# Optimization experiments

Hardware: AMD Instinct MI355X
Metric: run time of the kernel (lower is better)

The kernel has to match this reference:

```python
import jax, jax.numpy as jnp
import numpy as np

N_NODES = 30000
N_EDGES = 480000
IN_SIZE = 256
EDGE_FEAT = 32
N_TOWERS = 4
DELTA = 2.5


def setup_inputs():
    key = jax.random.key(0)
    ks = jax.random.split(key, 8)
    T, d = N_TOWERS, IN_SIZE // N_TOWERS
    m_in = 2 * d + EDGE_FEAT                 # M: Linear(2*tower_in+edge_feat -> tower_in)
    u_in = (4 * 3 + 1) * d                   # U: Linear((n_agg*n_scaler+1)*tower_in -> tower_out)
    return {
        "n_feat": jax.random.normal(ks[0], (N_NODES, IN_SIZE), jnp.float32),
        "e_feat": jax.random.normal(ks[1], (N_EDGES, EDGE_FEAT), jnp.float32),
        "src": jax.random.randint(ks[2], (N_EDGES,), 0, N_NODES),
        "dst": jax.random.randint(ks[3], (N_EDGES,), 0, N_NODES),
        "M_w": jax.random.normal(ks[4], (T, d, m_in), jnp.float32) * (1.0 / np.sqrt(m_in)),
        "M_b": jnp.zeros((T, d), jnp.float32),
        "U_w": jax.random.normal(ks[5], (T, d, u_in), jnp.float32) * (1.0 / np.sqrt(u_in)),
        "U_b": jnp.zeros((T, d), jnp.float32),
        "bn_gamma": jnp.ones((T, d), jnp.float32),
        "bn_beta": jnp.zeros((T, d), jnp.float32),
        "mix_w": jax.random.normal(ks[6], (IN_SIZE, IN_SIZE), jnp.float32) * (1.0 / np.sqrt(IN_SIZE)),
        "mix_b": jnp.zeros((IN_SIZE,), jnp.float32),
    }


def reference(n_feat, e_feat, src, dst, M_w, M_b, U_w, U_b, bn_gamma, bn_beta, mix_w, mix_b):
    N, F = n_feat.shape
    T, d, _ = M_w.shape
    E = src.shape[0]
    h = n_feat.reshape(N, T, d)                                   # towers split the feature dim
    ef = jnp.broadcast_to(e_feat[:, None, :], (E, T, e_feat.shape[1]))
    f = jnp.concatenate([h[src], h[dst], ef], axis=-1)            # [E,T,2d+ef]
    msg = jnp.einsum('eti,toi->eto', f, M_w) + M_b                # per-edge message, [E,T,d]

    deg = jax.ops.segment_sum(jnp.ones((E,), msg.dtype), dst, num_segments=N)  # in-degree
    degc = jnp.maximum(deg, 1.0)[:, None, None]
    s = jax.ops.segment_sum(msg, dst, num_segments=N)
    ssq = jax.ops.segment_sum(msg * msg, dst, num_segments=N)
    mean = s / degc
    var = jax.nn.relu(ssq / degc - mean * mean)                   # DGL aggregate_var
    std = jnp.sqrt(var + 1e-30)                                   # DGL aggregate_std
    has = (deg > 0.0)[:, None, None]
    mx = jnp.where(has, jax.ops.segment_max(msg, dst, num_segments=N), 0.0)
    mn = jnp.where(has, jax.ops.segment_min(msg, dst, num_segments=N), 0.0)
    agg = jnp.concatenate([mean, mx, mn, std], axis=-1)           # [N,T,4d]

    logd = jnp.log(deg + 1.0)
    amp = (logd / DELTA)[:, None, None]                            # amplification scaler
    att = jnp.where(deg > 0.0, DELTA / jnp.maximum(logd, 1e-12), 0.0)[:, None, None]  # attenuation
    hsc = jnp.concatenate([agg, agg * amp, agg * att], axis=-1)   # [N,T,12d]

    u_in = jnp.concatenate([h, hsc], axis=-1)                     # [N,T,13d]
    u = jnp.einsum('nti,toi->nto', u_in, U_w) + U_b               # [N,T,d]
    mu = jnp.mean(u, axis=0)
    v = jnp.mean((u - mu) ** 2, axis=0)
    u = (u - mu) / jnp.sqrt(v + 1e-5) * bn_gamma + bn_beta        # BatchNorm1d (training mode)

    h_cat = u.reshape(N, F)
    mixed = h_cat @ mix_w.T + mix_b
    mixed = jnp.where(mixed > 0, mixed, 0.01 * mixed)             # LeakyReLU mixing layer
    out = mixed + n_feat                                          # residual (in_size==out_size)
    return jax.nn.relu(out)                                       # last == 0 -> ReLU
```

## Files before the change

### kernel.cpp

```cpp
#include <hip/hip_runtime.h>
#include <math.h>

constexpr float DELTA_ = 2.5f;
#define BN_BLOCKS 512
#define NPB 8

typedef __attribute__((ext_vector_type(8))) short bf16x8;
typedef __attribute__((ext_vector_type(8))) _Float16 f16x8;
typedef __attribute__((ext_vector_type(4))) float f32x4;

__device__ inline ushort bf16h(float x){
  union { float f; unsigned u; } v; v.f = x;
  unsigned r = v.u + 0x7fffu + ((v.u >> 16) & 1u);
  return (ushort)(r >> 16);
}
__device__ inline float bf16f(ushort h){
  union { unsigned u; float f; } v; v.u = ((unsigned)h) << 16;
  return v.f;
}

__global__ __launch_bounds__(256) void k_tU(const float* __restrict__ Uw, ushort* __restrict__ Wpk2){
  int i = blockIdx.x*256 + threadIdx.x;
  if (i >= 4*192*320) return;
  int k   = i % 320;
  int col = (i/320) % 192;
  int t   = i/(320*192);
  int path = col >> 6, o = col & 63;
  float v = 0.f;
  int src = -1;
  if (k < 64){ if (path == 0) src = k; }
  else        src = k + path*256;
  if (src >= 0) v = Uw[((size_t)(t*64 + o))*832 + src];
  Wpk2[i] = bf16h(v);
}

__global__ __launch_bounds__(256) void k_tMm(const float* __restrict__ mixw, ushort* __restrict__ Wm2){
  int i = blockIdx.x*256 + threadIdx.x;
  if (i >= 256*256) return;
  Wm2[i] = bf16h(mixw[i]);
}

__global__ __launch_bounds__(256) void k_tW(const float* __restrict__ Mw, _Float16* __restrict__ Wall){
  int i = blockIdx.x*256 + threadIdx.x;
  if (i >= 4*4*3*64*8) return;
  int j     = i & 7;
  int lane  = (i >> 3) & 63;
  int slice = (i / 512) % 3;
  int cb    = (i / 1536) % 4;
  int t     = i / 6144;
  int ch = t*64 + cb*16 + (lane & 15);
  int k  = slice*32 + ((lane >> 4) & 3)*8 + j;
  int off = (k < 64) ? k : (128 + (k - 64));
  Wall[i] = (_Float16)Mw[(size_t)ch*160 + off];
}

__global__ __launch_bounds__(256) void k_hist(const int* __restrict__ dstv, int* __restrict__ cnt, int E){
  int e = blockIdx.x*256 + threadIdx.x;
  if (e < E) atomicAdd(&cnt[dstv[e]], 1);
}

__global__ __launch_bounds__(256) void k_scan1(const int* __restrict__ cnt, int* __restrict__ offs,
                                               int* __restrict__ bsum, int N){
  __shared__ int lds[256];
  int i = threadIdx.x;
  int g = blockIdx.x*256 + i;
  int v = (g < N) ? cnt[g] : 0;
  int acc = v;
  lds[i] = acc; __syncthreads();
  for (int s = 1; s < 256; s <<= 1){
    int t = (i >= s) ? lds[i - s] : 0;
    __syncthreads();
    acc += t; lds[i] = acc;
    __syncthreads();
  }
  if (g < N) offs[g] = acc - v;
  if (i == 255) bsum[blockIdx.x] = acc;
}

__global__ __launch_bounds__(256) void k_scan2(int* __restrict__ bsum, int NB){
  __shared__ int lds[256];
  int i = threadIdx.x;
  int v = (i < NB) ? bsum[i] : 0;
  int acc = v;
  lds[i] = acc; __syncthreads();
  for (int s = 1; s < 256; s <<= 1){
    int t = (i >= s) ? lds[i - s] : 0;
    __syncthreads();
    acc += t; lds[i] = acc;
    __syncthreads();
  }
  if (i < NB) bsum[i] = acc - v;
}

__global__ __launch_bounds__(256) void k_scan3(int* __restrict__ offs, const int* __restrict__ bsum, int N, int E){
  int g = blockIdx.x*256 + threadIdx.x;
  if (g < N) offs[g] += bsum[blockIdx.x];
  if (g == 0) offs[N] = E;
}

__global__ __launch_bounds__(256) void k_fill(const int* __restrict__ dstv, const int* __restrict__ offs,
                                              int* __restrict__ cur, int* __restrict__ elist, int E){
  int e = blockIdx.x*256 + threadIdx.x;
  if (e < E){
    int d = dstv[e];
    elist[offs[d] + atomicAdd(&cur[d], 1)] = e;
  }
}

__global__ __launch_bounds__(256) void k_perm(const int* __restrict__ elist, const int* __restrict__ srcv,
                                              const float* __restrict__ efeat,
                                              int* __restrict__ esrc, _Float16* __restrict__ efh, int E){
  int g = blockIdx.x*256 + threadIdx.x;
  int pos = g >> 3;
  int q   = g & 7;
  if (pos >= E) return;
  int e = elist[pos];
  if (q == 0) esrc[pos] = srcv[e];
  float4 v = *(const float4*)(efeat + (size_t)e*32 + q*4);
  union { ushort4 u; _Float16 h[4]; } cv;
  cv.h[0] = (_Float16)v.x; cv.h[1] = (_Float16)v.y;
  cv.h[2] = (_Float16)v.z; cv.h[3] = (_Float16)v.w;
  *(ushort4*)(efh + (size_t)pos*32 + q*4) = cv.u;
}

__global__ __launch_bounds__(256) void k_ab(const float* __restrict__ nf, const float* __restrict__ Mw,
                                            const float* __restrict__ Mb,
                                            _Float16* __restrict__ nfh, float* __restrict__ B,
                                            ushort* __restrict__ X2, int N){
  int c = threadIdx.x;
  int t = __builtin_amdgcn_readfirstlane(threadIdx.x >> 6);
  int d = c & 63;
  int jj = d >> 3, pp = d & 7;
  float wd[64];
  const float* row = Mw + (size_t)c*160 + 64;
#pragma unroll
  for (int k = 0; k < 64; k += 4){
    float4 b = *(const float4*)(row + k);
    wd[k]=b.x; wd[k+1]=b.y; wd[k+2]=b.z; wd[k+3]=b.w;
  }
  float bias = Mb[c];
  for (int n = blockIdx.x; n < N; n += gridDim.x){
    const float* h = nf + (size_t)n*256 + t*64;
    float sb = 0.f;
#pragma unroll
    for (int k = 0; k < 64; k += 4){
      float4 h4 = *(const float4*)(h + k);
      sb = fmaf(wd[k], h4.x, sb);
      sb = fmaf(wd[k+1], h4.y, sb);
      sb = fmaf(wd[k+2], h4.z, sb);
      sb = fmaf(wd[k+3], h4.w, sb);
    }
    B[(size_t)n*256 + c] = sb + bias;
    float v = nf[(size_t)n*256 + c];
    nfh[(size_t)n*256 + c] = (_Float16)v;
    ushort hi = bf16h(v);
    size_t base = (((size_t)n*4 + t)*40 + jj)*16;
    X2[base + pp]     = hi;
    X2[base + 8 + pp] = bf16h(v - bf16f(hi));
  }
}

__global__ __launch_bounds__(256) void k_agg(const int* __restrict__ offs, const int* __restrict__ esrc,
                                             const _Float16* __restrict__ efh,
                                             const _Float16* __restrict__ nfh, const float* __restrict__ B,
                                             const _Float16* __restrict__ Wall,
                                             ushort* __restrict__ X2, float* __restrict__ sc, int N, int E){
  __shared__ _Float16 eps[256][68];
  int tid = threadIdx.x;
  int lane = tid & 63, wv = tid >> 6;
  int li = lane & 15, kq = lane >> 4;
  int c = tid;
  int tw = c >> 6, d = c & 63;

  int n0 = blockIdx.x * NPB;
  if (n0 >= N) return;
  int n1 = n0 + NPB; if (n1 > N) n1 = N;
  int oS = offs[n0], oE = offs[n1];

  f16x8 bf[4][3];
#pragma unroll
  for (int cb = 0; cb < 4; ++cb)
#pragma unroll
    for (int sl = 0; sl < 3; ++sl)
      bf[cb][sl] = *(const f16x8*)(Wall + ((((size_t)wv*4 + cb)*3 + sl)*64 + lane)*8);

  int cur = n0;
  int curstart = oS;
  int nextoff = offs[n0 + 1];
  float s = 0.f, ss = 0.f;
  float mx = -__builtin_huge_valf(), mn = __builtin_huge_valf();

#define FINALIZE(CNT)                                                             \
  {                                                                                \
    float b = B[(size_t)cur*256 + c];                                              \
    float deg = (float)(CNT);                                                      \
    float degc = fmaxf(deg, 1.f);                                                  \
    float inv = 1.f / degc;                                                        \
    float S  = fmaf(deg, b, s);                                                    \
    float SS = fmaf(deg, b*b, fmaf(2.f*b, s, ss));                                 \
    float mean = S * inv;                                                          \
    float var  = fmaxf(SS * inv - mean*mean, 0.f);                                 \
    float sd   = sqrtf(var + 1e-30f);                                              \
    float MX = ((CNT) > 0) ? (b + mx) : 0.f;                                       \
    float MN = ((CNT) > 0) ? (b + mn) : 0.f;                                       \
    size_t xb = (((size_t)cur*4 + tw)*40)*16;                                      \
    { int kk = 64 + d;       ushort h2 = bf16h(mean);                              \
      X2[xb + (kk>>3)*16 + (kk&7)] = h2;                                           \
      X2[xb + (kk>>3)*16 + 8 + (kk&7)] = bf16h(mean - bf16f(h2)); }                \
    { int kk = 128 + d;      ushort h2 = bf16h(MX);                                \
      X2[xb + (kk>>3)*16 + (kk&7)] = h2;                                           \
      X2[xb + (kk>>3)*16 + 8 + (kk&7)] = bf16h(MX - bf16f(h2)); }                  \
    { int kk = 192 + d;      ushort h2 = bf16h(MN);                                \
      X2[xb + (kk>>3)*16 + (kk&7)] = h2;                                           \
      X2[xb + (kk>>3)*16 + 8 + (kk&7)] = bf16h(MN - bf16f(h2)); }                  \
    { int kk = 256 + d;      ushort h2 = bf16h(sd);                                \
      X2[xb + (kk>>3)*16 + (kk&7)] = h2;                                           \
      X2[xb + (kk>>3)*16 + 8 + (kk&7)] = bf16h(sd - bf16f(h2)); }                  \
    if (tid == 0){                                                                 \
      float logd = logf(deg + 1.f);                                                \
      sc[(size_t)cur*2]     = logd * (1.f / DELTA_);                               \
      sc[(size_t)cur*2 + 1] = ((CNT) > 0) ? (DELTA_ / fmaxf(logd, 1e-12f)) : 0.f;  \
    }                                                                              \
  }

  for (int w0 = oS; w0 < oE; w0 += 64){
    __syncthreads();
#pragma unroll
    for (int ch4 = 0; ch4 < 4; ++ch4){
      int pos = w0 + ch4*16 + li; if (pos > E - 1) pos = E - 1;
      int src = esrc[pos];
      const _Float16* hp = nfh + (size_t)src*256 + wv*64;
      f16x8 a0 = *(const f16x8*)(hp + kq*8);
      f16x8 a1 = *(const f16x8*)(hp + 32 + kq*8);
      f16x8 a2 = *(const f16x8*)(efh + (size_t)pos*32 + kq*8);
#pragma unroll
      for (int cb = 0; cb < 4; ++cb){
        f32x4 acc = __builtin_amdgcn_mfma_f32_16x16x32_f16(a0, bf[cb][0], (f32x4)0.f, 0, 0, 0);
        acc = __builtin_amdgcn_mfma_f32_16x16x32_f16(a1, bf[cb][1], acc, 0, 0, 0);
        acc = __builtin_amdgcn_mfma_f32_16x16x32_f16(a2, bf[cb][2], acc, 0, 0, 0);
        union { ushort4 u4; _Float16 h[4]; } st;
        st.h[0] = (_Float16)acc[0];
        st.h[1] = (_Float16)acc[1];
        st.h[2] = (_Float16)acc[2];
        st.h[3] = (_Float16)acc[3];
        *(ushort4*)(&eps[wv*64 + cb*16 + li][ch4*16 + kq*4]) = st.u4;
      }
    }
    __syncthreads();

    int wend = w0 + 64; if (wend > oE) wend = oE;
    for (int g = 0; g < 64; g += 4){
      if (w0 + g >= wend) break;
      union { ushort4 u4; _Float16 h[4]; } ld;
      ld.u4 = *(const ushort4*)(&eps[c][g]);
#pragma unroll
      for (int r = 0; r < 4; ++r){
        int idx = w0 + g + r;
        if (idx >= wend) break;
        while (idx == nextoff){
          FINALIZE(nextoff - curstart)
          curstart = nextoff;
          ++cur;
          nextoff = offs[cur + 1];
          s = 0.f; ss = 0.f;
          mx = -__builtin_huge_valf(); mn = __builtin_huge_valf();
        }
        float m = (float)ld.h[r];
        s += m;
        ss = fmaf(m, m, ss);
        mx = fmaxf(mx, m);
        mn = fminf(mn, m);
      }
    }
  }

  while (cur < n1){
    FINALIZE(nextoff - curstart)
    curstart = nextoff;
    ++cur;
    if (cur < n1) nextoff = offs[cur + 1];
    s = 0.f; ss = 0.f;
    mx = -__builtin_huge_valf(); mn = __builtin_huge_valf();
  }
#undef FINALIZE
}

__global__ __launch_bounds__(256) void k_u(const ushort* __restrict__ X2, const ushort* __restrict__ Wpk2,
                                           const float* __restrict__ sc, const float* __restrict__ Ub,
                                           float* __restrict__ uout, int Nn){
  __shared__ float su[64][68];
  int tid = threadIdx.x;
  int t   = blockIdx.y;
  int nbase = blockIdx.x*64;
  int lane = tid & 63, wv = tid >> 6;
  int li = lane & 15, kc = lane >> 4;
  int cbase = wv*48;

  f32x4 acc[4][3];
#pragma unroll
  for (int ri = 0; ri < 4; ++ri)
#pragma unroll
    for (int ci = 0; ci < 3; ++ci) acc[ri][ci] = (f32x4)0.f;

  const ushort* wb = Wpk2 + (size_t)t*192*320;

#pragma unroll 2
  for (int kt = 0; kt < 10; ++kt){
    bf16x8 ah[4], al[4], bh[3];
#pragma unroll
    for (int ri = 0; ri < 4; ++ri){
      int row = nbase + ri*16 + li;
      if (row >= Nn) row = Nn - 1;
      const ushort* ap = X2 + (((size_t)row*4 + t)*40 + kt*4 + kc)*16;
      ah[ri] = *(const bf16x8*)(ap);
      al[ri] = *(const bf16x8*)(ap + 8);
    }
#pragma unroll
    for (int ci = 0; ci < 3; ++ci){
      int col = cbase + ci*16 + li;
      bh[ci] = *(const bf16x8*)(wb + (size_t)col*320 + kt*32 + kc*8);
    }
#pragma unroll
    for (int ci = 0; ci < 3; ++ci)
#pragma unroll
      for (int ri = 0; ri < 4; ++ri){
        acc[ri][ci] = __builtin_amdgcn_mfma_f32_16x16x32_bf16(ah[ri], bh[ci], acc[ri][ci], 0, 0, 0);
        acc[ri][ci] = __builtin_amdgcn_mfma_f32_16x16x32_bf16(al[ri], bh[ci], acc[ri][ci], 0, 0, 0);
      }
  }

#define Y1_STORE(CI, OB) { _Pragma("unroll") for (int ri = 0; ri < 4; ++ri)               \
    { _Pragma("unroll") for (int r = 0; r < 4; ++r)                                        \
      su[ri*16 + kc*4 + r][(OB) + li] = acc[ri][CI][r]; } }
#define Y_ADD(CI, OB, SCOFF) { _Pragma("unroll") for (int ri = 0; ri < 4; ++ri)           \
    { _Pragma("unroll") for (int r = 0; r < 4; ++r){                                       \
      int node = ri*16 + kc*4 + r;                                                        \
      int gn = nbase + node; int gnc = (gn < Nn) ? gn : (Nn - 1);                          \
      float scl = sc[(size_t)gnc*2 + (SCOFF)];                                            \
      su[node][(OB) + li] += scl * acc[ri][CI][r]; } } }

  if (wv == 0){ Y1_STORE(0, 0)  Y1_STORE(1, 16) Y1_STORE(2, 32) }
  else if (wv == 1){ Y1_STORE(0, 48) }
  __syncthreads();
  if (wv == 1){ Y_ADD(1, 0, 0)  Y_ADD(2, 16, 0) }
  else if (wv == 2){ Y_ADD(0, 32, 0) Y_ADD(1, 48, 0) }
  __syncthreads();
  if (wv == 2){ Y_ADD(2, 0, 1) }
  else if (wv == 3){ Y_ADD(0, 16, 1) Y_ADD(1, 32, 1) Y_ADD(2, 48, 1) }
  __syncthreads();
#undef Y1_STORE
#undef Y_ADD

  for (int idx = tid; idx < 64*16; idx += 256){
    int n = idx >> 4, o4 = (idx & 15)*4;
    int gn = nbase + n;
    if (gn < Nn){
      float4 v = *(float4*)(&su[n][o4]);
      const float* ubp = Ub + t*64 + o4;
      v.x += ubp[0]; v.y += ubp[1]; v.z += ubp[2]; v.w += ubp[3];
      *(float4*)(&uout[(size_t)gn*256 + t*64 + o4]) = v;
    }
  }
}

__global__ __launch_bounds__(256) void k_bnstat(const float* __restrict__ u, float* __restrict__ part, int N){
  int c = threadIdx.x;
  int b = blockIdx.x;
  float s = 0.f, ss = 0.f;
  for (int n = b; n < N; n += gridDim.x){
    float v = u[(size_t)n*256 + c];
    s += v;
    ss = fmaf(v, v, ss);
  }
  part[(size_t)b*512 + c]       = s;
  part[(size_t)b*512 + 256 + c] = ss;
}

__global__ __launch_bounds__(256) void k_bnfin(const float* __restrict__ part, const float* __restrict__ gam,
                                               const float* __restrict__ bet, float* __restrict__ bnsc, int N){
  int c = threadIdx.x;
  float s = 0.f, ss = 0.f;
  for (int b = 0; b < BN_BLOCKS; ++b){
    s  += part[(size_t)b*512 + c];
    ss += part[(size_t)b*512 + 256 + c];
  }
  float invN = 1.f / (float)N;
  float mu  = s * invN;
  float ex2 = ss * invN;
  float var = fmaxf(ex2 - mu*mu, 0.f);
  float inv = 1.f / sqrtf(var + 1e-5f);
  float scale = gam[c] * inv;
  bnsc[c]       = scale;
  bnsc[256 + c] = bet[c] - mu*scale;
}

__global__ __launch_bounds__(256) void k_mix(const float* __restrict__ u, const ushort* __restrict__ Wm2,
                                             const float* __restrict__ bnsc,
                                             const float* __restrict__ mixb, const float* __restrict__ nf,
                                             float* __restrict__ outp, int Nn){
  int tid = threadIdx.x;
  int nbase = blockIdx.x*64;
  int lane = tid & 63, wv = tid >> 6;
  int li = lane & 15, kc = lane >> 4;

  f32x4 acc[4][4];
#pragma unroll
  for (int ri = 0; ri < 4; ++ri)
#pragma unroll
    for (int ci = 0; ci < 4; ++ci) acc[ri][ci] = (f32x4)0.f;

#pragma unroll 2
  for (int kt = 0; kt < 8; ++kt){
    int k0 = kt*32 + kc*8;
    float4 s40 = *(const float4*)(bnsc + k0);
    float4 s41 = *(const float4*)(bnsc + k0 + 4);
    float4 h40 = *(const float4*)(bnsc + 256 + k0);
    float4 h41 = *(const float4*)(bnsc + 256 + k0 + 4);
    bf16x8 ah[4], al[4], bh[4];
#pragma unroll
    for (int ri = 0; ri < 4; ++ri){
      int row = nbase + ri*16 + li;
      if (row >= Nn) row = Nn - 1;
      const float* up = u + (size_t)row*256 + k0;
      float4 v0 = *(const float4*)(up);
      float4 v1 = *(const float4*)(up + 4);
      float x[8];
      x[0] = fmaf(v0.x, s40.x, h40.x); x[1] = fmaf(v0.y, s40.y, h40.y);
      x[2] = fmaf(v0.z, s40.z, h40.z); x[3] = fmaf(v0.w, s40.w, h40.w);
      x[4] = fmaf(v1.x, s41.x, h41.x); x[5] = fmaf(v1.y, s41.y, h41.y);
      x[6] = fmaf(v1.z, s41.z, h41.z); x[7] = fmaf(v1.w, s41.w, h41.w);
      union { bf16x8 v; ushort u[8]; } hh, ll;
#pragma unroll
      for (int q = 0; q < 8; ++q){
        ushort hb = bf16h(x[q]);
        hh.u[q] = hb;
        ll.u[q] = bf16h(x[q] - bf16f(hb));
      }
      ah[ri] = hh.v;
      al[ri] = ll.v;
    }
#pragma unroll
    for (int ci = 0; ci < 4; ++ci){
      int col = wv*64 + ci*16 + li;
      bh[ci] = *(const bf16x8*)(Wm2 + (size_t)col*256 + kt*32 + kc*8);
    }
#pragma unroll
    for (int ci = 0; ci < 4; ++ci)
#pragma unroll
      for (int ri = 0; ri < 4; ++ri){
        acc[ri][ci] = __builtin_amdgcn_mfma_f32_16x16x32_bf16(ah[ri], bh[ci], acc[ri][ci], 0, 0, 0);
        acc[ri][ci] = __builtin_amdgcn_mfma_f32_16x16x32_bf16(al[ri], bh[ci], acc[ri][ci], 0, 0, 0);
      }
  }

  __syncthreads();
#pragma unroll
  for (int ri = 0; ri < 4; ++ri){
#pragma unroll
    for (int r = 0; r < 4; ++r){
      int node = ri*16 + kc*4 + r;
      int gn = nbase + node;
      if (gn < Nn){
#pragma unroll
        for (int ci = 0; ci < 4; ++ci){
          int col = wv*64 + ci*16 + li;
          float m = acc[ri][ci][r] + mixb[col];
          m = (m > 0.f) ? m : 0.01f*m;
          float o = m + nf[(size_t)gn*256 + col];
          outp[(size_t)gn*256 + col] = fmaxf(o, 0.f);
        }
      }
    }
  }
}

extern "C" void kernel_launch(void* const* d_in, const int* in_sizes, int n_in,
                              void* d_out, int out_size, void* d_ws, size_t ws_size,
                              hipStream_t stream){
  const float* nf   = (const float*)d_in[0];
  const float* ef   = (const float*)d_in[1];
  const int*   srcv = (const int*)  d_in[2];
  const int*   dstv = (const int*)  d_in[3];
  const float* Mw   = (const float*)d_in[4];
  const float* Mb   = (const float*)d_in[5];
  const float* Uw   = (const float*)d_in[6];
  const float* Ub   = (const float*)d_in[7];
  const float* gam  = (const float*)d_in[8];
  const float* bet  = (const float*)d_in[9];
  const float* mixw = (const float*)d_in[10];
  const float* mixb = (const float*)d_in[11];
  int N = in_sizes[0] / 256;
  int E = in_sizes[2];
  float* out = (float*)d_out;

  char* wp = (char*)d_ws;
  auto alloc = [&](size_t bytes){
    char* p = wp;
    wp += (bytes + 1023) & ~(size_t)1023;
    return (void*)p;
  };
  int*      cnt   = (int*)     alloc((size_t)N*4);
  int*      offs  = (int*)     alloc((size_t)(N+1)*4);
  int*      cur   = (int*)     alloc((size_t)N*4);
  int*      bsum  = (int*)     alloc(256*4);
  int*      elist = (int*)     alloc((size_t)E*4);
  int*      esrc  = (int*)     alloc((size_t)E*4);
  _Float16* efh   = (_Float16*)alloc((size_t)E*32*2);
  _Float16* nfh   = (_Float16*)alloc((size_t)N*256*2);
  float*    B     = (float*)   alloc((size_t)N*256*4);
  float*    sc    = (float*)   alloc((size_t)N*2*4);
  float*    part  = (float*)   alloc((size_t)BN_BLOCKS*512*4);
  float*    bnsc  = (float*)   alloc(512*4);
  ushort*   X2    = (ushort*)  alloc((size_t)N*4*40*16*2);
  ushort*   Wpk2  = (ushort*)  alloc((size_t)4*192*320*2);
  ushort*   Wm2   = (ushort*)  alloc((size_t)256*256*2);
  _Float16* Wall  = (_Float16*)alloc((size_t)4*4*3*64*8*2);

  hipMemsetAsync(cnt,  0, (size_t)N*4,  stream);
  hipMemsetAsync(cur,  0, (size_t)N*4,  stream);

  k_tU  <<<(4*192*320 + 255)/256, 256, 0, stream>>>(Uw, Wpk2);
  k_tMm <<<(256*256 + 255)/256, 256, 0, stream>>>(mixw, Wm2);
  k_tW  <<<(4*4*3*64*8 + 255)/256, 256, 0, stream>>>(Mw, Wall);
  k_hist<<<(E + 255)/256, 256, 0, stream>>>(dstv, cnt, E);
  k_ab  <<<2048, 256, 0, stream>>>(nf, Mw, Mb, nfh, B, X2, N);

  int NB = (N + 255)/256;
  k_scan1<<<NB, 256, 0, stream>>>(cnt, offs, bsum, N);
  k_scan2<<<1, 256, 0, stream>>>(bsum, NB);
  k_scan3<<<NB, 256, 0, stream>>>(offs, bsum, N, E);
  k_fill <<<(E + 255)/256, 256, 0, stream>>>(dstv, offs, cur, elist, E);
  k_perm <<<(E*8 + 255)/256, 256, 0, stream>>>(elist, srcv, ef, esrc, efh, E);

  k_agg<<<(N + NPB - 1)/NPB, 256, 0, stream>>>(offs, esrc, efh, nfh, B, Wall, X2, sc, N, E);

  dim3 ugrid((N + 63)/64, 4);
  k_u<<<ugrid, 256, 0, stream>>>(X2, Wpk2, sc, Ub, out, N);

  k_bnstat<<<BN_BLOCKS, 256, 0, stream>>>(out, part, N);
  k_bnfin <<<1, 256, 0, stream>>>(part, gam, bet, bnsc, N);
  k_mix  <<<(N + 63)/64, 256, 0, stream>>>(out, Wm2, bnsc, mixb, nf, out, N);
}
```

Before: 450.3 us.

## Fuse batchnorm partial statistics into the U-projection epilogue and double nodes per aggregation block

Per-block channel sums and sums of squares are computed from the shared-memory tile in k_u and written as partials. This removes the separate k_bnstat kernel that re-read the whole u tensor from global memory. k_bnfin now reduces these per-tile partials, one per 64-node block. Separately, the aggregation kernel now processes 16 nodes per block instead of 8, which changes its grid size and load balance.

```diff
diff --git a/kernel.cpp b/kernel.cpp
--- a/kernel.cpp
+++ b/kernel.cpp
@@ -2,8 +2,7 @@
 #include <math.h>
 
 constexpr float DELTA_ = 2.5f;
-#define BN_BLOCKS 512
-#define NPB 8
+#define NPB 16
 
 typedef __attribute__((ext_vector_type(8))) short bf16x8;
 typedef __attribute__((ext_vector_type(8))) _Float16 f16x8;
@@ -287,8 +286,10 @@
 
 __global__ __launch_bounds__(256) void k_u(const ushort* __restrict__ X2, const ushort* __restrict__ Wpk2,
                                            const float* __restrict__ sc, const float* __restrict__ Ub,
-                                           float* __restrict__ uout, int Nn){
+                                           float* __restrict__ uout, float* __restrict__ part,
+                                           int Nn, int NBLK){
   __shared__ float su[64][68];
+  __shared__ float pbn[2][4][64];
   int tid = threadIdx.x;
   int t   = blockIdx.y;
   int nbase = blockIdx.x*64;
@@ -361,28 +362,41 @@
       *(float4*)(&uout[(size_t)gn*256 + t*64 + o4]) = v;
     }
   }
-}
-
-__global__ __launch_bounds__(256) void k_bnstat(const float* __restrict__ u, float* __restrict__ part, int N){
+
+  {
+    int cl = tid & 63, grp = tid >> 6;
+    float ubv = Ub[t*64 + cl];
+    float ps = 0.f, pss = 0.f;
+#pragma unroll
+    for (int q = 0; q < 16; ++q){
+      int nn = grp*16 + q;
+      if (nbase + nn < Nn){
+        float v = su[nn][cl] + ubv;
+        ps += v;
+        pss = fmaf(v, v, pss);
+      }
+    }
+    pbn[0][grp][cl] = ps;
+    pbn[1][grp][cl] = pss;
+  }
+  __syncthreads();
+  if (tid < 128){
+    int which = tid >> 6, cl = tid & 63;
+    float v = pbn[which][0][cl] + pbn[which][1][cl] + pbn[which][2][cl] + pbn[which][3][cl];
+    part[((size_t)t*NBLK + blockIdx.x)*128 + which*64 + cl] = v;
+  }
+}
+
+__global__ __launch_bounds__(256) void k_bnfin(const float* __restrict__ part, const float* __restrict__ gam,
+                                               const float* __restrict__ bet, float* __restrict__ bnsc,
+                                               int N, int NBLK){
   int c = threadIdx.x;
-  int b = blockIdx.x;
+  int t = c >> 6, cl = c & 63;
   float s = 0.f, ss = 0.f;
-  for (int n = b; n < N; n += gridDim.x){
-    float v = u[(size_t)n*256 + c];
-    s += v;
-    ss = fmaf(v, v, ss);
-  }
-  part[(size_t)b*512 + c]       = s;
-  part[(size_t)b*512 + 256 + c] = ss;
-}
-
-__global__ __launch_bounds__(256) void k_bnfin(const float* __restrict__ part, const float* __restrict__ gam,
-                                               const float* __restrict__ bet, float* __restrict__ bnsc, int N){
-  int c = threadIdx.x;
-  float s = 0.f, ss = 0.f;
-  for (int b = 0; b < BN_BLOCKS; ++b){
-    s  += part[(size_t)b*512 + c];
-    ss += part[(size_t)b*512 + 256 + c];
+  for (int b = 0; b < NBLK; ++b){
+    const float* pp = part + ((size_t)t*NBLK + b)*128;
+    s  += pp[cl];
+    ss += pp[64 + cl];
   }
   float invN = 1.f / (float)N;
   float mu  = s * invN;
@@ -492,6 +506,7 @@
   int N = in_sizes[0] / 256;
   int E = in_sizes[2];
   float* out = (float*)d_out;
+  int NBLK = (N + 63)/64;
 
   char* wp = (char*)d_ws;
   auto alloc = [&](size_t bytes){
@@ -509,7 +524,7 @@
   _Float16* nfh   = (_Float16*)alloc((size_t)N*256*2);
   float*    B     = (float*)   alloc((size_t)N*256*4);
   float*    sc    = (float*)   alloc((size_t)N*2*4);
-  float*    part  = (float*)   alloc((size_t)BN_BLOCKS*512*4);
+  float*    part  = (float*)   alloc((size_t)4*NBLK*128*4);
   float*    bnsc  = (float*)   alloc(512*4);
   ushort*   X2    = (ushort*)  alloc((size_t)N*4*40*16*2);
   ushort*   Wpk2  = (ushort*)  alloc((size_t)4*192*320*2);
@@ -534,10 +549,9 @@
 
   k_agg<<<(N + NPB - 1)/NPB, 256, 0, stream>>>(offs, esrc, efh, nfh, B, Wall, X2, sc, N, E);
 
-  dim3 ugrid((N + 63)/64, 4);
-  k_u<<<ugrid, 256, 0, stream>>>(X2, Wpk2, sc, Ub, out, N);
-
-  k_bnstat<<<BN_BLOCKS, 256, 0, stream>>>(out, part, N);
-  k_bnfin <<<1, 256, 0, stream>>>(part, gam, bet, bnsc, N);
-  k_mix  <<<(N + 63)/64, 256, 0, stream>>>(out, Wm2, bnsc, mixb, nf, out, N);
-}
+  dim3 ugrid(NBLK, 4);
+  k_u<<<ugrid, 256, 0, stream>>>(X2, Wpk2, sc, Ub, out, part, N, NBLK);
+
+  k_bnfin<<<1, 256, 0, stream>>>(part, gam, bet, bnsc, N, NBLK);
+  k_mix  <<<NBLK, 256, 0, stream>>>(out, Wm2, bnsc, mixb, nf, out, N);
+}
```

Result: slower. 543.9 us (+20.8%).
